# Kernel optimization log

Measured on AMD Instinct MI355X. Metric: run time of the kernel, lower is better.

Reference implementation:

```python
import jax, jax.numpy as jnp
import numpy as np

# OpenCV GaussianBlur with ksize=3, sigma=0 uses the fixed small-kernel table
# [0.25, 0.5, 0.25] (separable), with border mode BORDER_REFLECT_101, which
# corresponds to jnp.pad(mode='reflect').
K0, K1 = 0.25, 0.5

def setup_inputs() -> dict:
    key = jax.random.key(0)
    x = jax.random.normal(key, (64, 3, 512, 512), dtype=jnp.float32)
    return {"x": x}

def _blur(x):
    # x: [B, C, H, W]; separable 1-2-1 / 4 filter along H then W.
    xp = jnp.pad(x, ((0, 0), (0, 0), (1, 1), (0, 0)), mode='reflect')
    x = K0 * xp[:, :, :-2, :] + K1 * xp[:, :, 1:-1, :] + K0 * xp[:, :, 2:, :]
    xp = jnp.pad(x, ((0, 0), (0, 0), (0, 0), (1, 1)), mode='reflect')
    x = K0 * xp[:, :, :, :-2] + K1 * xp[:, :, :, 1:-1] + K0 * xp[:, :, :, 2:]
    return x

def reference(x):
    return _blur(x)
```

## Files before the change

kernel.cpp:

```cpp
#include <hip/hip_runtime.h>


#define HH 512
#define WW 512

#define VBLUR(d, m, c, pq)                         \
    d.x = 0.25f * (m.x + pq.x) + 0.5f * c.x;       \
    d.y = 0.25f * (m.y + pq.y) + 0.5f * c.y;       \
    d.z = 0.25f * (m.z + pq.z) + 0.5f * c.z;       \
    d.w = 0.25f * (m.w + pq.w) + 0.5f * c.w;

#define HBLUR(oa, ob, ua, ub, l, r)                        \
    oa.x = 0.25f * (l    + ua.y) + 0.5f * ua.x;            \
    oa.y = 0.25f * (ua.x + ua.z) + 0.5f * ua.y;            \
    oa.z = 0.25f * (ua.y + ua.w) + 0.5f * ua.z;            \
    oa.w = 0.25f * (ua.z + ub.x) + 0.5f * ua.w;            \
    ob.x = 0.25f * (ua.w + ub.y) + 0.5f * ub.x;            \
    ob.y = 0.25f * (ub.x + ub.z) + 0.5f * ub.y;            \
    ob.z = 0.25f * (ub.y + ub.w) + 0.5f * ub.z;            \
    ob.w = 0.25f * (ub.z + r   ) + 0.5f * ub.w;

__global__ __launch_bounds__(256) void gauss3_kernel(const float* __restrict__ in,
                                                     float* __restrict__ out) {
    int wid  = (blockIdx.x * 256 + threadIdx.x) >> 6;
    int lane = threadIdx.x & 63;

    int rowpair = wid & 255;
    int plane   = wid >> 8;

    int h0 = rowpair << 1;
    int h1 = h0 + 1;
    int hm = (h0 == 0)      ? 1      : h0 - 1;
    int hp = (h1 == HH - 1) ? HH - 2 : h1 + 1;

    const float* p = in  + (size_t)plane * (HH * WW);
    float*       q = out + (size_t)plane * (HH * WW);
    int w0 = lane << 3;

    const float4* Lm = (const float4*)(p + (size_t)hm * WW + w0);
    const float4* L0 = (const float4*)(p + (size_t)h0 * WW + w0);
    const float4* L1 = (const float4*)(p + (size_t)h1 * WW + w0);
    const float4* Lp = (const float4*)(p + (size_t)hp * WW + w0);

    float4 am0 = Lm[0], am1 = Lm[1];
    float4 a00 = L0[0], a01 = L0[1];
    float4 a10 = L1[0], a11 = L1[1];
    float4 ap0 = Lp[0], ap1 = Lp[1];

    float4 u0a, u0b, u1a, u1b;
    VBLUR(u0a, am0, a00, a10)
    VBLUR(u0b, am1, a01, a11)
    VBLUR(u1a, a00, a10, ap0)
    VBLUR(u1b, a01, a11, ap1)

    float l0 = __shfl_up(u0b.w, 1);
    float l1 = __shfl_up(u1b.w, 1);
    float r0 = __shfl_down(u0a.x, 1);
    float r1 = __shfl_down(u1a.x, 1);
    if (lane == 0)  { l0 = u0a.y; l1 = u1a.y; }
    if (lane == 63) { r0 = u0b.z; r1 = u1b.z; }

    float4 o0a, o0b, o1a, o1b;
    HBLUR(o0a, o0b, u0a, u0b, l0, r0)
    HBLUR(o1a, o1b, u1a, u1b, l1, r1)

    float4* S0 = (float4*)(q + (size_t)h0 * WW + w0);
    float4* S1 = (float4*)(q + (size_t)h1 * WW + w0);
    S0[0] = o0a; S0[1] = o0b;
    S1[0] = o1a; S1[1] = o1b;
}

extern "C" void kernel_launch(void* const* d_in, const int* in_sizes, int n_in,
                              void* d_out, int out_size, void* d_ws, size_t ws_size,
                              hipStream_t stream) {
    const float* x   = (const float*)d_in[0];
    float*       out = (float*)d_out;

    int n      = in_sizes[0];
    int planes = n / (HH * WW);
    int waves  = planes * (HH / 2);
    int blocks = waves / 4;

    gauss3_kernel<<<blocks, 256, 0, stream>>>(x, out);
}
```

Baseline: 80.78 us.

## Process four rows per wave and use nontemporal stores for output

Each wavefront now handles four output rows instead of two, loading six input rows rather than four. This cuts halo re-reads from 2x to 1.5x of the input traffic. Output writes switch to nontemporal stores so they avoid polluting cache. The trade-off is fewer waves in flight and more registers per thread, which may reduce memory-level parallelism.

```diff
diff --git a/kernel.cpp b/kernel.cpp
--- a/kernel.cpp
+++ b/kernel.cpp
@@ -3,6 +3,8 @@
 
 #define HH 512
 #define WW 512
+
+typedef float f4 __attribute__((ext_vector_type(4)));
 
 #define VBLUR(d, m, c, pq)                         \
     d.x = 0.25f * (m.x + pq.x) + 0.5f * c.x;       \
@@ -10,64 +12,68 @@
     d.z = 0.25f * (m.z + pq.z) + 0.5f * c.z;       \
     d.w = 0.25f * (m.w + pq.w) + 0.5f * c.w;
 
-#define HBLUR(oa, ob, ua, ub, l, r)                        \
-    oa.x = 0.25f * (l    + ua.y) + 0.5f * ua.x;            \
-    oa.y = 0.25f * (ua.x + ua.z) + 0.5f * ua.y;            \
-    oa.z = 0.25f * (ua.y + ua.w) + 0.5f * ua.z;            \
-    oa.w = 0.25f * (ua.z + ub.x) + 0.5f * ua.w;            \
-    ob.x = 0.25f * (ua.w + ub.y) + 0.5f * ub.x;            \
-    ob.y = 0.25f * (ub.x + ub.z) + 0.5f * ub.y;            \
-    ob.z = 0.25f * (ub.y + ub.w) + 0.5f * ub.z;            \
+#define HBLUR(oa, ob, ua, ub, l, r)                \
+    oa.x = 0.25f * (l    + ua.y) + 0.5f * ua.x;    \
+    oa.y = 0.25f * (ua.x + ua.z) + 0.5f * ua.y;    \
+    oa.z = 0.25f * (ua.y + ua.w) + 0.5f * ua.z;    \
+    oa.w = 0.25f * (ua.z + ub.x) + 0.5f * ua.w;    \
+    ob.x = 0.25f * (ua.w + ub.y) + 0.5f * ub.x;    \
+    ob.y = 0.25f * (ub.x + ub.z) + 0.5f * ub.y;    \
+    ob.z = 0.25f * (ub.y + ub.w) + 0.5f * ub.z;    \
     ob.w = 0.25f * (ub.z + r   ) + 0.5f * ub.w;
+
+#define ROW_FINISH(ua, ub, h)                                        \
+    {                                                                \
+        float l = __shfl_up(ub.w, 1);                                \
+        float r = __shfl_down(ua.x, 1);                              \
+        if (lane == 0)  l = ua.y;                                    \
+        if (lane == 63) r = ub.z;                                    \
+        f4 oa, ob;                                                   \
+        HBLUR(oa, ob, ua, ub, l, r)                                  \
+        f4* S = (f4*)(q + (size_t)(h) * WW + w0);                    \
+        __builtin_nontemporal_store(oa, S);                          \
+        __builtin_nontemporal_store(ob, S + 1);                      \
+    }
 
 __global__ __launch_bounds__(256) void gauss3_kernel(const float* __restrict__ in,
                                                      float* __restrict__ out) {
     int wid  = (blockIdx.x * 256 + threadIdx.x) >> 6;
     int lane = threadIdx.x & 63;
 
-    int rowpair = wid & 255;
-    int plane   = wid >> 8;
+    int quad  = wid & 127;
+    int plane = wid >> 7;
 
-    int h0 = rowpair << 1;
-    int h1 = h0 + 1;
-    int hm = (h0 == 0)      ? 1      : h0 - 1;
-    int hp = (h1 == HH - 1) ? HH - 2 : h1 + 1;
+    int h0 = quad << 2;
+    int hm = (h0 == 0)       ? 1      : h0 - 1;
+    int hp = (h0 + 4 == HH)  ? HH - 2 : h0 + 4;
 
     const float* p = in  + (size_t)plane * (HH * WW);
     float*       q = out + (size_t)plane * (HH * WW);
     int w0 = lane << 3;
 
-    const float4* Lm = (const float4*)(p + (size_t)hm * WW + w0);
-    const float4* L0 = (const float4*)(p + (size_t)h0 * WW + w0);
-    const float4* L1 = (const float4*)(p + (size_t)h1 * WW + w0);
-    const float4* Lp = (const float4*)(p + (size_t)hp * WW + w0);
+    const f4* Lm = (const f4*)(p + (size_t)hm       * WW + w0);
+    const f4* L0 = (const f4*)(p + (size_t)h0       * WW + w0);
+    const f4* L1 = (const f4*)(p + (size_t)(h0 + 1) * WW + w0);
+    const f4* L2 = (const f4*)(p + (size_t)(h0 + 2) * WW + w0);
+    const f4* L3 = (const f4*)(p + (size_t)(h0 + 3) * WW + w0);
+    const f4* Lp = (const f4*)(p + (size_t)hp       * WW + w0);
 
-    float4 am0 = Lm[0], am1 = Lm[1];
-    float4 a00 = L0[0], a01 = L0[1];
-    float4 a10 = L1[0], a11 = L1[1];
-    float4 ap0 = Lp[0], ap1 = Lp[1];
+    f4 ama = Lm[0], amb = Lm[1];
+    f4 a0a = L0[0], a0b = L0[1];
+    f4 a1a = L1[0], a1b = L1[1];
+    f4 a2a = L2[0], a2b = L2[1];
+    f4 a3a = L3[0], a3b = L3[1];
+    f4 apa = Lp[0], apb = Lp[1];
 
-    float4 u0a, u0b, u1a, u1b;
-    VBLUR(u0a, am0, a00, a10)
-    VBLUR(u0b, am1, a01, a11)
-    VBLUR(u1a, a00, a10, ap0)
-    VBLUR(u1b, a01, a11, ap1)
-
-    float l0 = __shfl_up(u0b.w, 1);
-    float l1 = __shfl_up(u1b.w, 1);
-    float r0 = __shfl_down(u0a.x, 1);
-    float r1 = __shfl_down(u1a.x, 1);
-    if (lane == 0)  { l0 = u0a.y; l1 = u1a.y; }
-    if (lane == 63) { r0 = u0b.z; r1 = u1b.z; }
-
-    float4 o0a, o0b, o1a, o1b;
-    HBLUR(o0a, o0b, u0a, u0b, l0, r0)
-    HBLUR(o1a, o1b, u1a, u1b, l1, r1)
-
-    float4* S0 = (float4*)(q + (size_t)h0 * WW + w0);
-    float4* S1 = (float4*)(q + (size_t)h1 * WW + w0);
-    S0[0] = o0a; S0[1] = o0b;
-    S1[0] = o1a; S1[1] = o1b;
+    f4 ua, ub;
+    VBLUR(ua, ama, a0a, a1a)  VBLUR(ub, amb, a0b, a1b)
+    ROW_FINISH(ua, ub, h0)
+    VBLUR(ua, a0a, a1a, a2a)  VBLUR(ub, a0b, a1b, a2b)
+    ROW_FINISH(ua, ub, h0 + 1)
+    VBLUR(ua, a1a, a2a, a3a)  VBLUR(ub, a1b, a2b, a3b)
+    ROW_FINISH(ua, ub, h0 + 2)
+    VBLUR(ua, a2a, a3a, apa)  VBLUR(ub, a2b, a3b, apb)
+    ROW_FINISH(ua, ub, h0 + 3)
 }
 
 extern "C" void kernel_launch(void* const* d_in, const int* in_sizes, int n_in,
@@ -78,7 +84,7 @@
 
     int n      = in_sizes[0];
     int planes = n / (HH * WW);
-    int waves  = planes * (HH / 2);
+    int waves  = planes * (HH / 4);
     int blocks = waves / 4;
 
     gauss3_kernel<<<blocks, 256, 0, stream>>>(x, out);
```

Measured after the change: 76.40 us. 1.06x faster.
